# Kernel optimization log

Measured on AMD Instinct MI355X. Metric: run time of the kernel, lower is better.

Reference implementation:

```python
import jax, jax.numpy as jnp
import numpy as np

N, E, B = 50000, 800000, 1000
NODE_DIN, BB_DOUT, DHID, K = 32, 64, 64, 3
GLOB_DIN, EMBED_DIN = 64, 64
CIN = BB_DOUT + NODE_DIN  # 96


def setup_inputs() -> dict:
    key = jax.random.key(0)
    ks = jax.random.split(key, 24)

    def w(k, shape, fan_in):
        return jax.random.normal(k, shape, jnp.float32) / np.float32(np.sqrt(fan_in))

    inp = dict(
        x=jax.random.normal(ks[0], (N, NODE_DIN), jnp.float32),
        u=jax.random.normal(ks[1], (B, GLOB_DIN), jnp.float32),
        z=jax.random.normal(ks[2], (N, BB_DOUT), jnp.float32),
        edge_index=jax.random.randint(ks[3], (2, E), 0, N),
        edge_weight=jax.random.uniform(ks[4], (E,), jnp.float32),
        batch=jnp.sort(jax.random.randint(ks[5], (N,), 0, B)),
        batch_size=B,
        prev_h=jax.random.normal(ks[6], (N, DHID), jnp.float32),
    )
    # six ChebConvs of GConvGRU: x-convs take CIN, h-convs take DHID; all output DHID
    for i, nm in enumerate(["xz", "hz", "xr", "hr", "xh", "hh"]):
        cin = CIN if nm[0] == "x" else DHID
        inp[f"W{nm}"] = w(ks[7 + 2 * i], (K, cin, DHID), cin * K)
        inp[f"b{nm}"] = jnp.zeros((DHID,), jnp.float32)
    inp["Wg"] = w(ks[20], (GLOB_DIN, EMBED_DIN), GLOB_DIN)
    inp["bg"] = jnp.zeros((EMBED_DIN,), jnp.float32)
    return inp


def _cheb(xin, W, b, src, dst, w_norm, n):
    """ChebConv with sym norm, lambda_max=2 -> L_hat = -D^-1/2 A D^-1/2 (diag cancels)."""
    def prop(t):  # L_hat @ t  ([N,C])
        return -jax.ops.segment_sum(w_norm[:, None] * t[src], dst, num_segments=n)

    out = xin @ W[0] + b
    tx_prev = xin
    tx = None
    if W.shape[0] > 1:
        tx = prop(xin)
        out = out + tx @ W[1]
    for k in range(2, W.shape[0]):
        tx_new = 2.0 * prop(tx) - tx_prev
        out = out + tx_new @ W[k]
        tx_prev, tx = tx, tx_new
    return out


def reference(x, u, z, edge_index, edge_weight, batch, batch_size, prev_h,
              Wxz, bxz, Whz, bhz, Wxr, bxr, Whr, bhr, Wxh, bxh, Whh, bhh, Wg, bg):
    n = x.shape[0]
    src, dst = edge_index[0], edge_index[1]
    deg = jax.ops.segment_sum(edge_weight, src, num_segments=n)
    deg_safe = jnp.where(deg > 0, deg, 1.0)
    dinv = jnp.where(deg > 0, jax.lax.rsqrt(deg_safe), 0.0)
    w_norm = dinv[src] * edge_weight * dinv[dst]

    xin = jnp.concatenate([z, x], axis=-1)  # [N, CIN]
    Z = jax.nn.sigmoid(_cheb(xin, Wxz, bxz, src, dst, w_norm, n)
                       + _cheb(prev_h, Whz, bhz, src, dst, w_norm, n))
    R = jax.nn.sigmoid(_cheb(xin, Wxr, bxr, src, dst, w_norm, n)
                       + _cheb(prev_h, Whr, bhr, src, dst, w_norm, n))
    Ht = jnp.tanh(_cheb(xin, Wxh, bxh, src, dst, w_norm, n)
                  + _cheb(prev_h * R, Whh, bhh, src, dst, w_norm, n))
    h = Z * prev_h + (1.0 - Z) * Ht

    graph_emb = jax.ops.segment_sum(z, batch, num_segments=batch_size)  # [B, BB_DOUT]
    global_emb = jax.nn.relu(u @ Wg + bg)                                # [B, EMBED_DIN]
    fused = jnp.concatenate([graph_emb, global_emb], axis=-1)           # [B, 128]
    return fused, h
```

## Files before the change

kernel.cpp:

```cpp
#include <hip/hip_runtime.h>

#define NN 50000
#define EE 800000
#define BB 1000
#define NB 196
#define NR 5
#define RS 10496
#define NC 32
#define CHUNK 25000

#define BUILDBLKS 15625
#define PACKBLKS 204
#define FINBLKS 782

typedef unsigned short u16;
typedef __attribute__((ext_vector_type(8))) short bf16x8;
typedef __attribute__((ext_vector_type(4))) float f32x4;

static __device__ __forceinline__ u16 f2b(float f) {
    union { float f; unsigned u; } v;
    v.f = f;
    unsigned r = v.u + 0x7fffu + ((v.u >> 16) & 1u);
    return (u16)(r >> 16);
}

static __device__ __forceinline__ float b2f(short s) {
    union { unsigned u; float f; } c;
    c.u = ((unsigned)(u16)s) << 16;
    return c.f;
}

__global__ __launch_bounds__(512) void k_hist(
    const int* __restrict__ src, const int* __restrict__ dst,
    const float* __restrict__ ew, float* __restrict__ deg_p,
    int* __restrict__ cnt_p, int* __restrict__ ctr) {
    __shared__ float sdeg[RS];
    __shared__ unsigned scnt2[RS / 2];
    if (blockIdx.x == 0 && threadIdx.x == 0) atomicExch(ctr, 0);
    int r = blockIdx.x % NR;
    int c = blockIdx.x / NR;
    int base = r * RS;
    for (int i = threadIdx.x; i < RS; i += 512) sdeg[i] = 0.f;
    for (int i = threadIdx.x; i < RS / 2; i += 512) scnt2[i] = 0u;
    __syncthreads();
    int e0 = c * CHUNK;
    for (int j = threadIdx.x; j < CHUNK; j += 512) {
        int e = e0 + j;
        int s = src[e], d = dst[e];
        int sl = s - base, dl = d - base;
        if ((unsigned)sl < RS) atomicAdd(&sdeg[sl], ew[e]);
        if ((unsigned)dl < RS) atomicAdd(&scnt2[dl >> 1], (dl & 1) ? 65536u : 1u);
    }
    __syncthreads();
    int lim = (NN - base < RS) ? (NN - base) : RS;
    for (int i = threadIdx.x; i < lim; i += 512) {
        deg_p[(size_t)c * NN + base + i] = sdeg[i];
        cnt_p[(size_t)c * NN + base + i] = (int)((scnt2[i >> 1] >> ((i & 1) * 16)) & 0xffffu);
    }
}

__global__ __launch_bounds__(512) void k_build(
    const float* __restrict__ z, const float* __restrict__ x,
    const float* __restrict__ ph, u16* __restrict__ A0,
    const float* __restrict__ Wxz, const float* __restrict__ Wxr,
    const float* __restrict__ Wxh, const float* __restrict__ Whz,
    const float* __restrict__ Whr, const float* __restrict__ Whh,
    u16* __restrict__ Wp, u16* __restrict__ W3p) {
    int bid = blockIdx.x;
    if (bid < BUILDBLKS) {
        int i = bid * 512 + threadIdx.x;
        int n = i / 160, c = i - n * 160;
        float v;
        if (c < 64) v = z[n * 64 + c];
        else if (c < 96) v = x[n * 32 + (c - 64)];
        else v = ph[n * 64 + (c - 96)];
        A0[(size_t)n * 160 + c] = f2b(v);
        return;
    }
    int idx = (bid - BUILDBLKS) * 512 + threadIdx.x;
    if (idx < 15 * 12 * 512) {
        int j = idx & 7, l = (idx >> 3) & 63;
        int ct = (idx >> 9) % 12, s = (idx >> 9) / 12;
        int k = 32 * s + (l >> 4) * 8 + j;
        int g = ct >> 2;
        int c = 16 * (ct & 3) + (l & 15);
        int lvl = k / 160, kk = k - lvl * 160;
        float val;
        if (kk < 96) {
            const float* W = (g == 0) ? Wxz : ((g == 1) ? Wxr : Wxh);
            if (lvl == 0)      val = W[kk * 64 + c] - W[(192 + kk) * 64 + c];
            else if (lvl == 1) val = W[(96 + kk) * 64 + c];
            else               val = 2.f * W[(192 + kk) * 64 + c];
        } else if (g == 2) {
            val = 0.f;
        } else {
            const float* W = (g == 0) ? Whz : Whr;
            int kh = kk - 96;
            if (lvl == 0)      val = W[kh * 64 + c] - W[(128 + kh) * 64 + c];
            else if (lvl == 1) val = W[(64 + kh) * 64 + c];
            else               val = 2.f * W[(128 + kh) * 64 + c];
        }
        Wp[idx] = f2b(val);
    } else {
        int i2 = idx - 15 * 12 * 512;
        int j = i2 & 7, l = (i2 >> 3) & 63;
        int ct = (i2 >> 9) & 3, s = i2 >> 11;
        int k = 32 * s + (l >> 4) * 8 + j;
        int ki = k >> 6, kr = k & 63;
        int c = 16 * ct + (l & 15);
        float val;
        if (ki == 0)      val = Whh[kr * 64 + c] - Whh[(128 + kr) * 64 + c];
        else if (ki == 1) val = Whh[(64 + kr) * 64 + c];
        else              val = 2.f * Whh[(128 + kr) * 64 + c];
        W3p[i2] = f2b(val);
    }
}

__global__ __launch_bounds__(256) void k_scan(
    const int* __restrict__ cnt_p, const float* __restrict__ deg_p,
    int* __restrict__ cnt, int* __restrict__ cbase, float* __restrict__ dinv,
    int* __restrict__ bsum, int* __restrict__ ctr) {
    __shared__ int s[256];
    int b = blockIdx.x;
    int i = b * 256 + threadIdx.x;
    int cp[NC];
    int v = 0;
    float d = 0.f;
    if (i < NN) {
#pragma unroll
        for (int p = 0; p < NC; p++) {
            cp[p] = cnt_p[(size_t)p * NN + i];
            v += cp[p];
            d += deg_p[(size_t)p * NN + i];
        }
        cnt[i] = v;
    }
    s[threadIdx.x] = v;
    __syncthreads();
    for (int off = 1; off < 256; off <<= 1) {
        int t = (threadIdx.x >= off) ? s[threadIdx.x - off] : 0;
        __syncthreads();
        s[threadIdx.x] += t;
        __syncthreads();
    }
    int incl = s[threadIdx.x];
    if (threadIdx.x == 255) atomicExch(&bsum[b], s[255]);
    __threadfence();
    if (threadIdx.x == 0) {
        atomicAdd(ctr, 1);
        while (atomicAdd(ctr, 0) < NB) __builtin_amdgcn_s_sleep(8);
    }
    __syncthreads();
    __threadfence();
    int pv = (threadIdx.x < b) ? atomicAdd(&bsum[threadIdx.x], 0) : 0;
    s[threadIdx.x] = pv;
    __syncthreads();
    for (int off = 128; off > 0; off >>= 1) {
        if (threadIdx.x < off) s[threadIdx.x] += s[threadIdx.x + off];
        __syncthreads();
    }
    int prefix = s[0];
    if (i < NN) {
        int run = prefix + incl - v;
        dinv[i] = d > 0.f ? rsqrtf(d) : 0.f;
#pragma unroll
        for (int c = 0; c < NC; c++) {
            cbase[(size_t)c * NN + i] = run;
            run += cp[c];
        }
    }
}

__global__ __launch_bounds__(512) void k_scatter_rank(
    const int* __restrict__ src, const int* __restrict__ dst,
    const float* __restrict__ ew, const float* __restrict__ dinv,
    const int* __restrict__ cbase, uint2* __restrict__ csr8) {
    __shared__ unsigned rank2[RS / 2];
    int r = blockIdx.x % NR;
    int c = blockIdx.x / NR;
    int base = r * RS;
    for (int i = threadIdx.x; i < RS / 2; i += 512) rank2[i] = 0u;
    __syncthreads();
    int e0 = c * CHUNK;
    for (int j = threadIdx.x; j < CHUNK; j += 512) {
        int e = e0 + j;
        int d = dst[e];
        int dl = d - base;
        if ((unsigned)dl < RS) {
            int s = src[e];
            unsigned old = atomicAdd(&rank2[dl >> 1], (dl & 1) ? 65536u : 1u);
            int rank = (int)((old >> ((dl & 1) * 16)) & 0xffffu);
            int pos = cbase[(size_t)c * NN + d] + rank;
            float w = dinv[s] * ew[e] * dinv[d];
            csr8[pos] = make_uint2((unsigned)s, __float_as_uint(w));
        }
    }
}

template <int C, int BS, int INS, int OUTS>
__global__ __launch_bounds__(BS) void k_pull(
    const u16* __restrict__ in, u16* __restrict__ out,
    const uint2* __restrict__ csr8, const int* __restrict__ row_ptr,
    const int* __restrict__ cnt) {
    constexpr int TPR = C / 16;
    int tid = blockIdx.x * BS + threadIdx.x;
    int r = tid / TPR;
    int c16 = (tid - r * TPR) * 16;
    if (r >= NN) return;
    int s0 = row_ptr[r], n = cnt[r];
    float acc[16];
#pragma unroll
    for (int k = 0; k < 16; k++) acc[k] = 0.f;
    const u16* inp = in + c16;
    uint2 e = (n > 0) ? csr8[s0] : make_uint2(0u, 0u);
    for (int j = 0; j < n; j++) {
        uint2 ec = e;
        if (j + 1 < n) e = csr8[s0 + j + 1];
        float w = __uint_as_float(ec.y);
        const u16* p = inp + (size_t)ec.x * INS;
        bf16x8 v0 = *(const bf16x8*)(p);
        bf16x8 v1 = *(const bf16x8*)(p + 8);
#pragma unroll
        for (int k = 0; k < 8; k++) {
            acc[k] += w * b2f(v0[k]);
            acc[8 + k] += w * b2f(v1[k]);
        }
    }
    bf16x8 p0, p1;
#pragma unroll
    for (int k = 0; k < 8; k++) {
        p0[k] = (short)f2b(-acc[k]);
        p1[k] = (short)f2b(-acc[8 + k]);
    }
    u16* op = out + (size_t)r * OUTS + c16;
    *(bf16x8*)(op) = p0;
    *(bf16x8*)(op + 8) = p1;
}

__global__ __launch_bounds__(256) void k_gates_mfma(
    const u16* __restrict__ A0, const u16* __restrict__ A1, const u16* __restrict__ A2,
    const u16* __restrict__ Wp,
    const float* __restrict__ bxz, const float* __restrict__ bhz,
    const float* __restrict__ bxr, const float* __restrict__ bhr,
    const float* __restrict__ bxh,
    u16* __restrict__ Zb16, u16* __restrict__ Hx16, u16* __restrict__ A3) {
    int wv = (blockIdx.x * 256 + threadIdx.x) >> 6;
    int lane = threadIdx.x & 63;
    int r0 = wv * 16;
    if (r0 >= NN) return;
    int q = lane >> 4, j0 = lane & 15;

    f32x4 acc[12];
#pragma unroll
    for (int i = 0; i < 12; i++) acc[i] = (f32x4){0.f, 0.f, 0.f, 0.f};

    size_t rofs = (size_t)(r0 + j0) * 160 + q * 8;
    const u16* arow[3] = {A0 + rofs, A1 + rofs, A2 + rofs};
#pragma unroll
    for (int s = 0; s < 15; s++) {
        bf16x8 a = *(const bf16x8*)(arow[s / 5] + 32 * (s % 5));
        const u16* bp = Wp + (size_t)(s * 12) * 512 + lane * 8;
#pragma unroll
        for (int ct = 0; ct < 12; ct++) {
            bf16x8 b = *(const bf16x8*)(bp + ct * 512);
            acc[ct] = __builtin_amdgcn_mfma_f32_16x16x32_bf16(a, b, acc[ct], 0, 0, 0);
        }
    }

#pragma unroll
    for (int ct = 0; ct < 4; ct++) {
        int j = 16 * ct + j0;
        float bz = bxz[j] + bhz[j];
        float br = bxr[j] + bhr[j];
        float bh = bxh[j];
#pragma unroll
        for (int reg = 0; reg < 4; reg++) {
            int r = r0 + q * 4 + reg;
            size_t i = (size_t)r * 64 + j;
            float zp = acc[ct][reg] + bz;
            float rp = acc[ct + 4][reg] + br;
            float hp = acc[ct + 8][reg] + bh;
            float zv = 1.f / (1.f + expf(-zp));
            float rv = 1.f / (1.f + expf(-rp));
            float phv = b2f((short)A0[(size_t)r * 160 + 96 + j]);
            Zb16[i] = f2b(zv);
            Hx16[i] = f2b(hp);
            A3[(size_t)r * 192 + j] = f2b(rv * phv);
        }
    }
}

__global__ __launch_bounds__(256) void k_final_tail(
    const u16* __restrict__ A3, const u16* __restrict__ W3p,
    const float* __restrict__ bhh, const u16* __restrict__ Hx16,
    const u16* __restrict__ Zb16, const u16* __restrict__ A0,
    float* __restrict__ outh,
    const float* __restrict__ z, const int* __restrict__ batch,
    const float* __restrict__ u, const float* __restrict__ Wg,
    const float* __restrict__ bg, float* __restrict__ outF) {
    if (blockIdx.x >= FINBLKS) {
        int b = ((blockIdx.x - FINBLKS) * 256 + threadIdx.x) >> 6;
        int lane = threadIdx.x & 63;
        if (b >= BB) return;
        int lo = 0, hi = NN;
        while (lo < hi) {
            int m = (lo + hi) >> 1;
            if (batch[m] < b) lo = m + 1; else hi = m;
        }
        int start = lo;
        hi = NN;
        while (lo < hi) {
            int m = (lo + hi) >> 1;
            if (batch[m] < b + 1) lo = m + 1; else hi = m;
        }
        int end = lo;
        float acc = 0.f;
        for (int n = start; n < end; n++) acc += z[(size_t)n * 64 + lane];
        float g = bg[lane];
        const float* ur = u + (size_t)b * 64;
        for (int k = 0; k < 64; k++) g += ur[k] * Wg[k * 64 + lane];
        g = fmaxf(g, 0.f);
        outF[(size_t)b * 128 + lane] = acc;
        outF[(size_t)b * 128 + 64 + lane] = g;
        return;
    }
    int wv = (blockIdx.x * 256 + threadIdx.x) >> 6;
    int lane = threadIdx.x & 63;
    int r0 = wv * 16;
    if (r0 >= NN) return;
    int q = lane >> 4, j0 = lane & 15;

    f32x4 acc[4];
#pragma unroll
    for (int i = 0; i < 4; i++) acc[i] = (f32x4){0.f, 0.f, 0.f, 0.f};

    const u16* arow = A3 + (size_t)(r0 + j0) * 192 + q * 8;
#pragma unroll
    for (int s = 0; s < 6; s++) {
        bf16x8 a = *(const bf16x8*)(arow + 32 * s);
        const u16* bp = W3p + (size_t)(s * 4) * 512 + lane * 8;
#pragma unroll
        for (int ct = 0; ct < 4; ct++) {
            bf16x8 b = *(const bf16x8*)(bp + ct * 512);
            acc[ct] = __builtin_amdgcn_mfma_f32_16x16x32_bf16(a, b, acc[ct], 0, 0, 0);
        }
    }

#pragma unroll
    for (int ct = 0; ct < 4; ct++) {
        int j = 16 * ct + j0;
        float bh = bhh[j];
#pragma unroll
        for (int reg = 0; reg < 4; reg++) {
            int r = r0 + q * 4 + reg;
            size_t i = (size_t)r * 64 + j;
            float ht = tanhf(b2f((short)Hx16[i]) + acc[ct][reg] + bh);
            float zv = b2f((short)Zb16[i]);
            float phv = b2f((short)A0[(size_t)r * 160 + 96 + j]);
            outh[i] = zv * phv + (1.f - zv) * ht;
        }
    }
}

extern "C" void kernel_launch(void* const* d_in, const int* in_sizes, int n_in,
                              void* d_out, int out_size, void* d_ws, size_t ws_size,
                              hipStream_t stream) {
    const float* x  = (const float*)d_in[0];
    const float* u  = (const float*)d_in[1];
    const float* z  = (const float*)d_in[2];
    const int*   ei = (const int*)d_in[3];
    const float* ew = (const float*)d_in[4];
    const int* batch = (const int*)d_in[5];
    const float* ph = (const float*)d_in[7];
    const float *Wxz = (const float*)d_in[8],  *bxz = (const float*)d_in[9];
    const float *Whz = (const float*)d_in[10], *bhz = (const float*)d_in[11];
    const float *Wxr = (const float*)d_in[12], *bxr = (const float*)d_in[13];
    const float *Whr = (const float*)d_in[14], *bhr = (const float*)d_in[15];
    const float *Wxh = (const float*)d_in[16], *bxh = (const float*)d_in[17];
    const float *Whh = (const float*)d_in[18], *bhh = (const float*)d_in[19];
    const float *Wg  = (const float*)d_in[20], *bg  = (const float*)d_in[21];
    const int* src = ei;
    const int* dst = ei + EE;

    char* wsb = (char*)d_ws;
    size_t o = 0;
    auto alloc = [&](size_t bytes) {
        void* p = wsb + o;
        o += (bytes + 255) & ~(size_t)255;
        return p;
    };
    float* deg_p = (float*)alloc((size_t)NC * NN * 4);
    int*   cnt_p = (int*)alloc((size_t)NC * NN * 4);
    int*   cnt   = (int*)alloc(NN * 4);
    int*   cbase = (int*)alloc((size_t)NC * NN * 4);
    float* dinv  = (float*)alloc(NN * 4);
    int*   bsum  = (int*)alloc(256 * 4);
    int*   ctr   = (int*)alloc(256);
    uint2* csr8  = (uint2*)alloc((size_t)EE * 8);
    u16*   Zb16  = (u16*)alloc((size_t)NN * 64 * 2);
    u16*   Hx16  = (u16*)alloc((size_t)NN * 64 * 2);
    u16*   A0    = (u16*)alloc((size_t)NN * 160 * 2);
    u16*   A1    = (u16*)alloc((size_t)NN * 160 * 2);
    u16*   A2    = (u16*)alloc((size_t)NN * 160 * 2);
    u16*   A3    = (u16*)alloc((size_t)NN * 192 * 2);
    u16*   Wp    = (u16*)alloc(15 * 12 * 512 * 2);
    u16*   W3p   = (u16*)alloc(6 * 4 * 512 * 2);

    float* outF = (float*)d_out;
    float* outH = outF + (size_t)BB * 128;

    const int BLK = 256;
    const int gPull160 = (NN + 31) / 32;
    const int gPull64 = (NN + 63) / 64;
    const int gTail = (BB * 64 + BLK - 1) / BLK;
    int* row_ptr = cbase;

    k_hist<<<NR * NC, 512, 0, stream>>>(src, dst, ew, deg_p, cnt_p, ctr);

    k_build<<<BUILDBLKS + PACKBLKS, 512, 0, stream>>>(
        z, x, ph, A0, Wxz, Wxr, Wxh, Whz, Whr, Whh, Wp, W3p);

    k_scan<<<NB, 256, 0, stream>>>(cnt_p, deg_p, cnt, cbase, dinv, bsum, ctr);

    k_scatter_rank<<<NR * NC, 512, 0, stream>>>(src, dst, ew, dinv, cbase, csr8);

    k_pull<160, 320, 160, 160><<<gPull160, 320, 0, stream>>>(A0, A1, csr8, row_ptr, cnt);
    k_pull<160, 320, 160, 160><<<gPull160, 320, 0, stream>>>(A1, A2, csr8, row_ptr, cnt);

    k_gates_mfma<<<FINBLKS, BLK, 0, stream>>>(A0, A1, A2, Wp, bxz, bhz, bxr, bhr, bxh,
                                              Zb16, Hx16, A3);

    k_pull<64, 256, 192, 192><<<gPull64, 256, 0, stream>>>(A3, A3 + 64, csr8, row_ptr, cnt);
    k_pull<64, 256, 192, 192><<<gPull64, 256, 0, stream>>>(A3 + 64, A3 + 128, csr8, row_ptr, cnt);

    k_final_tail<<<FINBLKS + gTail, BLK, 0, stream>>>(A3, W3p, bhh, Hx16, Zb16, A0, outH,
                                                      z, batch, u, Wg, bg, outF);
}
```

Measured before the change: 449.3 us.

## Record per-edge rank during histogram and replace rank-scatter with flat edge scatter

```diff
diff --git a/kernel.cpp b/kernel.cpp
--- a/kernel.cpp
+++ b/kernel.cpp
@@ -33,7 +33,7 @@
 __global__ __launch_bounds__(512) void k_hist(
     const int* __restrict__ src, const int* __restrict__ dst,
     const float* __restrict__ ew, float* __restrict__ deg_p,
-    int* __restrict__ cnt_p, int* __restrict__ ctr) {
+    int* __restrict__ cnt_p, int* __restrict__ rank, int* __restrict__ ctr) {
     __shared__ float sdeg[RS];
     __shared__ unsigned scnt2[RS / 2];
     if (blockIdx.x == 0 && threadIdx.x == 0) atomicExch(ctr, 0);
@@ -49,7 +49,10 @@
         int s = src[e], d = dst[e];
         int sl = s - base, dl = d - base;
         if ((unsigned)sl < RS) atomicAdd(&sdeg[sl], ew[e]);
-        if ((unsigned)dl < RS) atomicAdd(&scnt2[dl >> 1], (dl & 1) ? 65536u : 1u);
+        if ((unsigned)dl < RS) {
+            unsigned old = atomicAdd(&scnt2[dl >> 1], (dl & 1) ? 65536u : 1u);
+            rank[e] = (int)((old >> ((dl & 1) * 16)) & 0xffffu);
+        }
     }
     __syncthreads();
     int lim = (NN - base < RS) ? (NN - base) : RS;
@@ -123,17 +126,16 @@
     __shared__ int s[256];
     int b = blockIdx.x;
     int i = b * 256 + threadIdx.x;
-    int cp[NC];
     int v = 0;
     float d = 0.f;
     if (i < NN) {
 #pragma unroll
         for (int p = 0; p < NC; p++) {
-            cp[p] = cnt_p[(size_t)p * NN + i];
-            v += cp[p];
+            v += cnt_p[(size_t)p * NN + i];
             d += deg_p[(size_t)p * NN + i];
         }
         cnt[i] = v;
+        dinv[i] = d > 0.f ? rsqrtf(d) : 0.f;
     }
     s[threadIdx.x] = v;
     __syncthreads();
@@ -162,39 +164,25 @@
     int prefix = s[0];
     if (i < NN) {
         int run = prefix + incl - v;
-        dinv[i] = d > 0.f ? rsqrtf(d) : 0.f;
 #pragma unroll
         for (int c = 0; c < NC; c++) {
             cbase[(size_t)c * NN + i] = run;
-            run += cp[c];
-        }
-    }
-}
-
-__global__ __launch_bounds__(512) void k_scatter_rank(
-    const int* __restrict__ src, const int* __restrict__ dst,
-    const float* __restrict__ ew, const float* __restrict__ dinv,
-    const int* __restrict__ cbase, uint2* __restrict__ csr8) {
-    __shared__ unsigned rank2[RS / 2];
-    int r = blockIdx.x % NR;
-    int c = blockIdx.x / NR;
-    int base = r * RS;
-    for (int i = threadIdx.x; i < RS / 2; i += 512) rank2[i] = 0u;
-    __syncthreads();
-    int e0 = c * CHUNK;
-    for (int j = threadIdx.x; j < CHUNK; j += 512) {
-        int e = e0 + j;
-        int d = dst[e];
-        int dl = d - base;
-        if ((unsigned)dl < RS) {
-            int s = src[e];
-            unsigned old = atomicAdd(&rank2[dl >> 1], (dl & 1) ? 65536u : 1u);
-            int rank = (int)((old >> ((dl & 1) * 16)) & 0xffffu);
-            int pos = cbase[(size_t)c * NN + d] + rank;
-            float w = dinv[s] * ew[e] * dinv[d];
-            csr8[pos] = make_uint2((unsigned)s, __float_as_uint(w));
-        }
-    }
+            run += cnt_p[(size_t)c * NN + i];
+        }
+    }
+}
+
+__global__ void k_scatter(const int* __restrict__ src, const int* __restrict__ dst,
+                          const float* __restrict__ ew, const float* __restrict__ dinv,
+                          const int* __restrict__ cbase, const int* __restrict__ rank,
+                          uint2* __restrict__ csr8) {
+    int e = blockIdx.x * 256 + threadIdx.x;
+    if (e >= EE) return;
+    int c = e / CHUNK;
+    int d = dst[e], s = src[e];
+    int pos = cbase[(size_t)c * NN + d] + rank[e];
+    float w = dinv[s] * ew[e] * dinv[d];
+    csr8[pos] = make_uint2((unsigned)s, __float_as_uint(w));
 }
 
 template <int C, int BS, int INS, int OUTS>
@@ -393,6 +381,7 @@
     int*   cnt_p = (int*)alloc((size_t)NC * NN * 4);
     int*   cnt   = (int*)alloc(NN * 4);
     int*   cbase = (int*)alloc((size_t)NC * NN * 4);
+    int*   rank  = (int*)alloc((size_t)EE * 4);
     float* dinv  = (float*)alloc(NN * 4);
     int*   bsum  = (int*)alloc(256 * 4);
     int*   ctr   = (int*)alloc(256);
@@ -410,19 +399,20 @@
     float* outH = outF + (size_t)BB * 128;
 
     const int BLK = 256;
+    const int gE = (EE + BLK - 1) / BLK;
     const int gPull160 = (NN + 31) / 32;
     const int gPull64 = (NN + 63) / 64;
     const int gTail = (BB * 64 + BLK - 1) / BLK;
     int* row_ptr = cbase;
 
-    k_hist<<<NR * NC, 512, 0, stream>>>(src, dst, ew, deg_p, cnt_p, ctr);
+    k_hist<<<NR * NC, 512, 0, stream>>>(src, dst, ew, deg_p, cnt_p, rank, ctr);
 
     k_build<<<BUILDBLKS + PACKBLKS, 512, 0, stream>>>(
         z, x, ph, A0, Wxz, Wxr, Wxh, Whz, Whr, Whh, Wp, W3p);
 
     k_scan<<<NB, 256, 0, stream>>>(cnt_p, deg_p, cnt, cbase, dinv, bsum, ctr);
 
-    k_scatter_rank<<<NR * NC, 512, 0, stream>>>(src, dst, ew, dinv, cbase, csr8);
+    k_scatter<<<gE, BLK, 0, stream>>>(src, dst, ew, dinv, cbase, rank, csr8);
 
     k_pull<160, 320, 160, 160><<<gPull160, 320, 0, stream>>>(A0, A1, csr8, row_ptr, cnt);
     k_pull<160, 320, 160, 160><<<gPull160, 320, 0, stream>>>(A1, A2, csr8, row_ptr, cnt);
```

Result: faster. 431.1 us (-4.0%).
